# Optimization experiments

Hardware: AMD Instinct MI355X
Metric: run time of the kernel (lower is better)

Reference implementation:

```python
import math
import jax, jax.numpy as jnp
import numpy as np

B, T, C, H = 4, 2048, 1024, 16
HD = C // H

def gelu_tanh(x):
    return 0.5 * x * (1.0 + jnp.tanh(jnp.sqrt(2.0 / jnp.pi) * (x + 0.044715 * x * x * x)))

def layernorm(x, w, b, eps=1e-5):
    mu = jnp.mean(x, axis=-1, keepdims=True)
    var = jnp.var(x, axis=-1, keepdims=True)
    return (x - mu) * jax.lax.rsqrt(var + eps) * w + b

def setup_inputs() -> dict:
    key = jax.random.key(0)
    ks = jax.random.split(key, 8)
    s = 0.02
    return {
        "x": jax.random.normal(ks[0], (B, T, C), dtype=jnp.float32),
        "ln1_w": jnp.ones((C,), jnp.float32), "ln1_b": jnp.zeros((C,), jnp.float32),
        "attn_w": jax.random.normal(ks[1], (C, 3 * C), jnp.float32) * s,
        "attn_b": jnp.zeros((3 * C,), jnp.float32),
        "proj_w": jax.random.normal(ks[2], (C, C), jnp.float32) * s,
        "proj_b": jnp.zeros((C,), jnp.float32),
        "ln2_w": jnp.ones((C,), jnp.float32), "ln2_b": jnp.zeros((C,), jnp.float32),
        "fc_w": jax.random.normal(ks[3], (C, 4 * C), jnp.float32) * s,
        "fc_b": jnp.zeros((4 * C,), jnp.float32),
        "fc_proj_w": jax.random.normal(ks[4], (4 * C, C), jnp.float32) * s,
        "fc_proj_b": jnp.zeros((C,), jnp.float32),
    }

def block(x, ln1_w, ln1_b, attn_w, attn_b, proj_w, proj_b,
          ln2_w, ln2_b, fc_w, fc_b, fc_proj_w, fc_proj_b):
    # --- causal self-attention ---
    h = layernorm(x, ln1_w, ln1_b)
    qkv = h @ attn_w + attn_b                      # [B,T,3C]
    q, k, v = jnp.split(qkv, 3, axis=-1)
    q = q.reshape(B, T, H, HD).transpose(0, 2, 1, 3)  # [B,H,T,hd]
    k = k.reshape(B, T, H, HD).transpose(0, 2, 1, 3)
    v = v.reshape(B, T, H, HD).transpose(0, 2, 1, 3)
    att = jnp.einsum('bhqd,bhkd->bhqk', q, k) * (1.0 / math.sqrt(HD))
    mask = jnp.tril(jnp.ones((T, T), dtype=bool))
    att = jnp.where(mask, att, -jnp.inf)
    att = jax.nn.softmax(att, axis=-1)
    y = jnp.einsum('bhqk,bhkd->bhqd', att, v)
    y = y.transpose(0, 2, 1, 3).reshape(B, T, C)
    x = x + (y @ proj_w + proj_b)
    # --- MLP ---
    h = layernorm(x, ln2_w, ln2_b)
    h = gelu_tanh(h @ fc_w + fc_b)
    x = x + (h @ fc_proj_w + fc_proj_b)
    return x

def reference(x, ln1_w, ln1_b, attn_w, attn_b, proj_w, proj_b,
              ln2_w, ln2_b, fc_w, fc_b, fc_proj_w, fc_proj_b):
    return block(x, ln1_w, ln1_b, attn_w, attn_b, proj_w, proj_b,
                 ln2_w, ln2_b, fc_w, fc_b, fc_proj_w, fc_proj_b)
```

## Files before the change

### kernel.cpp

```cpp
#include <hip/hip_runtime.h>
#include <stdint.h>

#define TSEQ 2048
#define CDIM 1024
#define NHEAD 16
#define HDIM 64
#define NROWS 8192

typedef __bf16 bf16x8 __attribute__((ext_vector_type(8)));
typedef float f32x4 __attribute__((ext_vector_type(4)));
typedef float f32x16 __attribute__((ext_vector_type(16)));

__device__ __forceinline__ unsigned short f2bf(float f) {
  unsigned u = __builtin_bit_cast(unsigned, f);
  u = u + 0x7fffu + ((u >> 16) & 1u);
  return (unsigned short)(u >> 16);
}

__device__ __forceinline__ unsigned cvt_pk_bf16(float a, float b) {
  unsigned r;
  asm("v_cvt_pk_bf16_f32 %0, %1, %2" : "=v"(r) : "v"(a), "v"(b));
  return r;
}

__device__ __forceinline__ float gelu_f(float x) {
  float x3 = x * x * x;
  float z = 0.7978845608028654f * (x + 0.044715f * x3);
  float e = __expf(2.f * z);
  float t = 1.f - 2.f / (e + 1.f);
  return 0.5f * x * (1.f + t);
}

__device__ __forceinline__ void ldg_lds16(void* lds, const void* gsrc) {
  __builtin_amdgcn_global_load_lds(
      (__attribute__((address_space(1))) unsigned int*)(uintptr_t)gsrc,
      (__attribute__((address_space(3))) unsigned int*)lds,
      16, 0, 0);
}

__global__ __launch_bounds__(256) void k_wtrans(const float* __restrict__ W,
                                                unsigned short* __restrict__ Wt,
                                                int K, int N) {
  __shared__ unsigned short tl[32][40];
  int n0 = blockIdx.x * 32, k0 = blockIdx.y * 32;
  int tid = threadIdx.x;
  int r = tid >> 3, c4 = (tid & 7) * 4;
  float4 v = *(const float4*)(W + (size_t)(k0 + r) * N + n0 + c4);
  ushort4 o;
  o.x = f2bf(v.x); o.y = f2bf(v.y); o.z = f2bf(v.z); o.w = f2bf(v.w);
  *(ushort4*)&tl[r][c4] = o;
  __syncthreads();
  int n = tid >> 3, k4 = (tid & 7) * 4;
  ushort4 w;
  w.x = tl[k4 + 0][n]; w.y = tl[k4 + 1][n]; w.z = tl[k4 + 2][n]; w.w = tl[k4 + 3][n];
  *(ushort4*)(Wt + (size_t)(n0 + n) * K + k0 + k4) = w;
}

__global__ __launch_bounds__(256) void k_ln(const float* __restrict__ x,
                                            const float* __restrict__ w,
                                            const float* __restrict__ b,
                                            unsigned short* __restrict__ out) {
  int row = blockIdx.x;
  int tid = threadIdx.x;
  const float* xr = x + (size_t)row * CDIM;
  float4 v = *(const float4*)(xr + tid * 4);
  float s = v.x + v.y + v.z + v.w;
  float s2 = v.x * v.x + v.y * v.y + v.z * v.z + v.w * v.w;
#pragma unroll
  for (int off = 32; off; off >>= 1) {
    s += __shfl_xor(s, off);
    s2 += __shfl_xor(s2, off);
  }
  __shared__ float rbuf[8];
  int wv = tid >> 6, lane = tid & 63;
  if (lane == 0) { rbuf[wv] = s; rbuf[4 + wv] = s2; }
  __syncthreads();
  float S1 = rbuf[0] + rbuf[1] + rbuf[2] + rbuf[3];
  float S2 = rbuf[4] + rbuf[5] + rbuf[6] + rbuf[7];
  float mean = S1 * (1.f / CDIM);
  float var = S2 * (1.f / CDIM) - mean * mean;
  float rstd = rsqrtf(var + 1e-5f);
  float4 wv4 = *(const float4*)(w + tid * 4);
  float4 bv4 = *(const float4*)(b + tid * 4);
  ushort4 o;
  o.x = f2bf((v.x - mean) * rstd * wv4.x + bv4.x);
  o.y = f2bf((v.y - mean) * rstd * wv4.y + bv4.y);
  o.z = f2bf((v.z - mean) * rstd * wv4.z + bv4.z);
  o.w = f2bf((v.w - mean) * rstd * wv4.w + bv4.w);
  *(ushort4*)(out + (size_t)row * CDIM + tid * 4) = o;
}

template <int EPI>
__global__ __launch_bounds__(512, 4)
void k_gemm(const unsigned short* __restrict__ A,
            const unsigned short* __restrict__ Bt,
            const float* __restrict__ bias,
            const float* __restrict__ resid,
            void* __restrict__ Cout,
            int M, int N, int K) {
  constexpr int ABYTES = 128 * 64;
  constexpr int BBYTES = 256 * 64;
  constexpr int BUFSZ = ABYTES + BBYTES;
  __shared__ __align__(16) char lds[3 * BUFSZ];
  const int tid = threadIdx.x;
  const int wid = tid >> 6, lane = tid & 63;
  const int wm = wid >> 2, wn = wid & 3;
  const int fr = lane & 15, fq = lane >> 4;

  const int gx = gridDim.x;
  int flat = blockIdx.y * gx + blockIdx.x;
  {
    const int nwg = gx * gridDim.y;
    int q = nwg >> 3, r = nwg & 7;
    int xcd = flat & 7, idx = flat >> 3;
    flat = (xcd < r ? xcd * (q + 1) : r * (q + 1) + (xcd - r) * q) + idx;
  }
  const int bx = flat % gx, by = flat / gx;
  const long brow = (long)by * 128, bcol = (long)bx * 256;

  const int sby = (((lane & 3) ^ ((lane >> 3) & 3)) << 4);
  const char* gA = (const char*)(A + (size_t)(brow + wid * 16 + (lane >> 2)) * K) + sby;
  const char* gB = (const char*)(Bt + (size_t)(bcol + wid * 32 + (lane >> 2)) * K) + sby;

  const int NT = K >> 5;

#define STAGE_A(tt, bf)                                                 \
  ldg_lds16(lds + (bf) * BUFSZ + wid * 1024, gA + (size_t)(tt) * 64)
#define STAGE_B(tt, bf)                                                 \
  do {                                                                  \
    char* d_ = lds + (bf) * BUFSZ + ABYTES + wid * 2048;                \
    ldg_lds16(d_, gB + (size_t)(tt) * 64);                              \
    ldg_lds16(d_ + 1024, gB + (size_t)16 * K * 2 + (size_t)(tt) * 64);  \
  } while (0)

  STAGE_A(0, 0); STAGE_B(0, 0);
  STAGE_A(1, 1); STAGE_B(1, 1);

  f32x4 acc[4][4];
  const f32x4 vzero = {0.f, 0.f, 0.f, 0.f};
#pragma unroll
  for (int m = 0; m < 4; ++m)
#pragma unroll
    for (int n = 0; n < 4; ++n) acc[m][n] = vzero;

  const int ksw = ((fq ^ ((fr >> 1) & 3)) << 4);
  int buf = 0;
  for (int t = 0; t < NT; ++t) {
    if (t + 1 < NT) asm volatile("s_waitcnt vmcnt(3)" ::: "memory");
    else            asm volatile("s_waitcnt vmcnt(0)" ::: "memory");
    __builtin_amdgcn_s_barrier();
    __builtin_amdgcn_sched_barrier(0);
    const char* pA = lds + buf * BUFSZ;
    const char* pB = pA + ABYTES;
    int nbuf = buf + 2; if (nbuf >= 3) nbuf -= 3;
    if (t + 2 < NT) { STAGE_A(t + 2, nbuf); STAGE_B(t + 2, nbuf); }
    bf16x8 af[4], bfr[4];
#pragma unroll
    for (int m = 0; m < 4; ++m)
      af[m] = *(const bf16x8*)(pA + (wm * 64 + m * 16 + fr) * 64 + ksw);
#pragma unroll
    for (int n = 0; n < 4; ++n)
      bfr[n] = *(const bf16x8*)(pB + (wn * 64 + n * 16 + fr) * 64 + ksw);
    __builtin_amdgcn_s_setprio(1);
#pragma unroll
    for (int m = 0; m < 4; ++m)
#pragma unroll
      for (int n = 0; n < 4; ++n)
        acc[m][n] = __builtin_amdgcn_mfma_f32_16x16x32_bf16(af[m], bfr[n], acc[m][n], 0, 0, 0);
    __builtin_amdgcn_s_setprio(0);
    __builtin_amdgcn_sched_barrier(0);
    buf = buf + 1; if (buf == 3) buf = 0;
  }
#undef STAGE_A
#undef STAGE_B

#pragma unroll
  for (int m = 0; m < 4; ++m) {
    long row = brow + wm * 64 + m * 16 + fq * 4;
#pragma unroll
    for (int n = 0; n < 4; ++n) {
      long col = bcol + wn * 64 + n * 16 + fr;
      float bv = bias[col];
#pragma unroll
      for (int r = 0; r < 4; ++r) {
        float v = acc[m][n][r] + bv;
        long idx = (row + r) * (long)N + col;
        if (EPI == 0) {
          ((unsigned short*)Cout)[idx] = f2bf(v);
        } else if (EPI == 1) {
          ((unsigned short*)Cout)[idx] = f2bf(gelu_f(v));
        } else {
          ((float*)Cout)[idx] = v + resid[idx];
        }
      }
    }
  }
}

__global__ __launch_bounds__(256) void k_build_vt(const unsigned short* __restrict__ qkv,
                                                  unsigned short* __restrict__ vt) {
  __shared__ __align__(16) unsigned short tl[64][80];
  int bh = blockIdx.x, b = bh >> 4, h = bh & 15;
  int t0 = blockIdx.y * 64;
  int tid = threadIdx.x;
  int r = tid >> 2, cb = (tid & 3) * 16;
  const unsigned short* src =
      qkv + (size_t)(b * TSEQ + t0 + r) * (3 * CDIM) + 2 * CDIM + h * HDIM + cb;
  *(uint4*)&tl[r][cb] = *(const uint4*)src;
  *(uint4*)&tl[r][cb + 8] = *(const uint4*)(src + 8);
  __syncthreads();
  int d = tid >> 2, tb = (tid & 3) * 16;
  union { unsigned short u[16]; uint4 v[2]; } o;
#pragma unroll
  for (int j = 0; j < 16; ++j) o.u[j] = tl[tb + j][d];
  unsigned short* dst = vt + ((size_t)bh * HDIM + d) * TSEQ + t0 + tb;
  *(uint4*)dst = o.v[0];
  *(uint4*)(dst + 8) = o.v[1];
}

struct QSt {
  f32x16 OTlo, OThi;
  float m, l;
};

__device__ __forceinline__ void attn_qk_sm_pv(
    const bf16x8& k0, const bf16x8& k1, const bf16x8& k2, const bf16x8& k3,
    const bf16x8& v0, const bf16x8& v1, const bf16x8& v2, const bf16x8& v3,
    const bf16x8& q0f, const bf16x8& q1f, const bf16x8& q2f, const bf16x8& q3f,
    QSt& S, bool diag, int lq, int hi) {
  const float SC = 0.125f * 1.44269504088896f;
  f32x16 st;
#pragma unroll
  for (int r = 0; r < 16; ++r) st[r] = 0.f;
  st = __builtin_amdgcn_mfma_f32_32x32x16_bf16(k0, q0f, st, 0, 0, 0);
  st = __builtin_amdgcn_mfma_f32_32x32x16_bf16(k1, q1f, st, 0, 0, 0);
  st = __builtin_amdgcn_mfma_f32_32x32x16_bf16(k2, q2f, st, 0, 0, 0);
  st = __builtin_amdgcn_mfma_f32_32x32x16_bf16(k3, q3f, st, 0, 0, 0);
#pragma unroll
  for (int r = 0; r < 16; ++r) st[r] *= SC;
  if (diag) {
#pragma unroll
    for (int r = 0; r < 16; ++r) {
      int kvl = (r & 3) + 8 * (r >> 2) + 4 * hi;
      if (kvl > lq) st[r] = -1e30f;
    }
  }
  float tmax = st[0];
#pragma unroll
  for (int r = 1; r < 16; ++r) tmax = fmaxf(tmax, st[r]);
  float tm = fmaxf(tmax, __shfl_xor(tmax, 32));
  if (__any(tm > S.m + 8.f)) {
    float mnew = fmaxf(S.m, tm);
    float alpha = __builtin_amdgcn_exp2f(S.m - mnew);
    S.m = mnew;
    S.OTlo *= alpha;
    S.OThi *= alpha;
    S.l *= alpha;
  }
  unsigned c[8];
  float rs = 0.f;
#pragma unroll
  for (int i = 0; i < 8; ++i) {
    float pa = __builtin_amdgcn_exp2f(st[2 * i] - S.m);
    float pb = __builtin_amdgcn_exp2f(st[2 * i + 1] - S.m);
    rs += pa + pb;
    c[i] = cvt_pk_bf16(pa, pb);
  }
  S.l += rs + __shfl_xor(rs, 32);
  unsigned pc[8];
#pragma unroll
  for (int i = 0; i < 8; ++i) pc[i] = __shfl_xor(c[i], 32);
  uint4 w1, w2;
  w1.x = hi ? pc[2] : c[0]; w1.y = hi ? pc[3] : c[1];
  w1.z = hi ? c[2] : pc[0]; w1.w = hi ? c[3] : pc[1];
  w2.x = hi ? pc[6] : c[4]; w2.y = hi ? pc[7] : c[5];
  w2.z = hi ? c[6] : pc[4]; w2.w = hi ? c[7] : pc[5];
  bf16x8 f1 = __builtin_bit_cast(bf16x8, w1);
  bf16x8 f2 = __builtin_bit_cast(bf16x8, w2);
  S.OTlo = __builtin_amdgcn_mfma_f32_32x32x16_bf16(v0, f1, S.OTlo, 0, 0, 0);
  S.OTlo = __builtin_amdgcn_mfma_f32_32x32x16_bf16(v1, f2, S.OTlo, 0, 0, 0);
  S.OThi = __builtin_amdgcn_mfma_f32_32x32x16_bf16(v2, f1, S.OThi, 0, 0, 0);
  S.OThi = __builtin_amdgcn_mfma_f32_32x32x16_bf16(v3, f2, S.OThi, 0, 0, 0);
}

__global__ __launch_bounds__(256, 2) void k_attn(const unsigned short* __restrict__ qkv,
                                                 const unsigned short* __restrict__ vt,
                                                 unsigned short* __restrict__ y) {
  __shared__ __align__(16) unsigned short Ks[2][2048];
  __shared__ __align__(16) unsigned short Vs[2][2048];
  const int bh = blockIdx.x, b = bh >> 4, h = bh & 15;
  const int wv = threadIdx.x >> 6, lane = threadIdx.x & 63;
  const int by = blockIdx.y;
  const int w = by * 4 + wv;
  const int lq = lane & 31, hi = lane >> 5;
  const int ntL = w, ntH = 63 - w;
  const int q0L = w * 32, q0H = (63 - w) * 32;
  const int T = 64 - 4 * by;

  const unsigned short* qrowL = qkv + ((size_t)(b * TSEQ) + q0L + lq) * (3 * CDIM) + h * HDIM;
  const unsigned short* qrowH = qkv + ((size_t)(b * TSEQ) + q0H + lq) * (3 * CDIM) + h * HDIM;
  bf16x8 qL0 = *(const bf16x8*)(qrowL + 0 + hi * 8);
  bf16x8 qL1 = *(const bf16x8*)(qrowL + 16 + hi * 8);
  bf16x8 qL2 = *(const bf16x8*)(qrowL + 32 + hi * 8);
  bf16x8 qL3 = *(const bf16x8*)(qrowL + 48 + hi * 8);
  bf16x8 qH0 = *(const bf16x8*)(qrowH + 0 + hi * 8);
  bf16x8 qH1 = *(const bf16x8*)(qrowH + 16 + hi * 8);
  bf16x8 qH2 = *(const bf16x8*)(qrowH + 32 + hi * 8);
  bf16x8 qH3 = *(const bf16x8*)(qrowH + 48 + hi * 8);

  const int kr = lane & 31, kc = wv * 2 + (lane >> 5);
  const unsigned short* gK =
      qkv + ((size_t)(b * TSEQ) + kr) * (3 * CDIM) + CDIM + h * HDIM + kc * 8;
  const unsigned short* gV = vt + ((size_t)bh * HDIM + lane) * TSEQ + wv * 8;

#define STAGEKV(bf_, tt)                                                  \
  do {                                                                    \
    ldg_lds16((char*)Ks[bf_] + wv * 1024, gK + (size_t)(tt) * 32 * (3 * CDIM)); \
    ldg_lds16((char*)Vs[bf_] + wv * 1024, gV + (tt) * 32);                \
  } while (0)

  QSt SL, SH;
#pragma unroll
  for (int r = 0; r < 16; ++r) {
    SL.OTlo[r] = 0.f; SL.OThi[r] = 0.f; SH.OTlo[r] = 0.f; SH.OThi[r] = 0.f;
  }
  SL.m = -1e30f; SL.l = 0.f; SH.m = -1e30f; SH.l = 0.f;

  STAGEKV(0, 0);
  for (int t = 0; t < T; ++t) {
    __syncthreads();
    if (t + 1 < T) STAGEKV((t + 1) & 1, t + 1);
    if (t <= ntH) {
      const unsigned short* Kb = Ks[t & 1];
      const unsigned short* Vb = Vs[t & 1];
      bf16x8 k0 = *(const bf16x8*)(Kb + (0 + hi) * 256 + lq * 8);
      bf16x8 k1 = *(const bf16x8*)(Kb + (2 + hi) * 256 + lq * 8);
      bf16x8 k2 = *(const bf16x8*)(Kb + (4 + hi) * 256 + lq * 8);
      bf16x8 k3 = *(const bf16x8*)(Kb + (6 + hi) * 256 + lq * 8);
      bf16x8 v0 = *(const bf16x8*)(Vb + hi * 512 + lq * 8);
      bf16x8 v1 = *(const bf16x8*)(Vb + (2 + hi) * 512 + lq * 8);
      bf16x8 v2 = *(const bf16x8*)(Vb + hi * 512 + (lq + 32) * 8);
      bf16x8 v3 = *(const bf16x8*)(Vb + (2 + hi) * 512 + (lq + 32) * 8);
      attn_qk_sm_pv(k0, k1, k2, k3, v0, v1, v2, v3,
                    qH0, qH1, qH2, qH3, SH, t == ntH, lq, hi);
      if (t <= ntL)
        attn_qk_sm_pv(k0, k1, k2, k3, v0, v1, v2, v3,
                      qL0, qL1, qL2, qL3, SL, t == ntL, lq, hi);
    }
  }
#undef STAGEKV

  {
    float inv = 1.f / SH.l;
    unsigned short* yrow = y + ((size_t)(b * TSEQ) + q0H + lq) * CDIM + h * HDIM;
#pragma unroll
    for (int r = 0; r < 16; r += 2) {
      int d = (r & 3) + 8 * (r >> 2) + 4 * hi;
      unsigned lo0 = f2bf(SH.OTlo[r] * inv), lo1 = f2bf(SH.OTlo[r + 1] * inv);
      *(unsigned*)(yrow + d) = lo0 | (lo1 << 16);
      unsigned h0 = f2bf(SH.OThi[r] * inv), h1 = f2bf(SH.OThi[r + 1] * inv);
      *(unsigned*)(yrow + 32 + d) = h0 | (h1 << 16);
    }
  }
  {
    float inv = 1.f / SL.l;
    unsigned short* yrow = y + ((size_t)(b * TSEQ) + q0L + lq) * CDIM + h * HDIM;
#pragma unroll
    for (int r = 0; r < 16; r += 2) {
      int d = (r & 3) + 8 * (r >> 2) + 4 * hi;
      unsigned lo0 = f2bf(SL.OTlo[r] * inv), lo1 = f2bf(SL.OTlo[r + 1] * inv);
      *(unsigned*)(yrow + d) = lo0 | (lo1 << 16);
      unsigned h0 = f2bf(SL.OThi[r] * inv), h1 = f2bf(SL.OThi[r + 1] * inv);
      *(unsigned*)(yrow + 32 + d) = h0 | (h1 << 16);
    }
  }
}

extern "C" void kernel_launch(void* const* d_in, const int* in_sizes, int n_in,
                              void* d_out, int out_size, void* d_ws, size_t ws_size,
                              hipStream_t stream) {
  const float* x = (const float*)d_in[0];
  const float* ln1_w = (const float*)d_in[1];
  const float* ln1_b = (const float*)d_in[2];
  const float* attn_w = (const float*)d_in[3];
  const float* attn_b = (const float*)d_in[4];
  const float* proj_w = (const float*)d_in[5];
  const float* proj_b = (const float*)d_in[6];
  const float* ln2_w = (const float*)d_in[7];
  const float* ln2_b = (const float*)d_in[8];
  const float* fc_w = (const float*)d_in[9];
  const float* fc_b = (const float*)d_in[10];
  const float* fc_proj_w = (const float*)d_in[11];
  const float* fc_proj_b = (const float*)d_in[12];

  char* ws = (char*)d_ws;
  unsigned short* wt_attn = (unsigned short*)(ws + 0);
  unsigned short* wt_proj = (unsigned short*)(ws + 6291456);
  unsigned short* wt_fc = (unsigned short*)(ws + 8388608);
  unsigned short* wt_fcp = (unsigned short*)(ws + 16777216);
  float* x1 = (float*)(ws + 25165824);
  unsigned short* hbuf = (unsigned short*)(ws + 58720256);
  unsigned short* ybuf = (unsigned short*)(ws + 75497472);
  unsigned short* qkvb = (unsigned short*)(ws + 92274688);
  unsigned short* vtb = (unsigned short*)(ws + 142606336);
  unsigned short* gbuf = (unsigned short*)(ws + 92274688);

  k_wtrans<<<dim3(3072 / 32, 1024 / 32), 256, 0, stream>>>(attn_w, wt_attn, 1024, 3072);
  k_wtrans<<<dim3(1024 / 32, 1024 / 32), 256, 0, stream>>>(proj_w, wt_proj, 1024, 1024);
  k_wtrans<<<dim3(4096 / 32, 1024 / 32), 256, 0, stream>>>(fc_w, wt_fc, 1024, 4096);
  k_wtrans<<<dim3(1024 / 32, 4096 / 32), 256, 0, stream>>>(fc_proj_w, wt_fcp, 4096, 1024);

  k_ln<<<NROWS, 256, 0, stream>>>(x, ln1_w, ln1_b, hbuf);

  k_gemm<0><<<dim3(3072 / 256, NROWS / 128), 512, 0, stream>>>(
      hbuf, wt_attn, attn_b, nullptr, qkvb, NROWS, 3072, 1024);

  k_build_vt<<<dim3(64, TSEQ / 64), 256, 0, stream>>>(qkvb, vtb);

  k_attn<<<dim3(64, 8), 256, 0, stream>>>(qkvb, vtb, ybuf);

  k_gemm<2><<<dim3(1024 / 256, NROWS / 128), 512, 0, stream>>>(
      ybuf, wt_proj, proj_b, x, x1, NROWS, 1024, 1024);

  k_ln<<<NROWS, 256, 0, stream>>>(x1, ln2_w, ln2_b, hbuf);

  k_gemm<1><<<dim3(4096 / 256, NROWS / 128), 512, 0, stream>>>(
      hbuf, wt_fc, fc_b, nullptr, gbuf, NROWS, 4096, 1024);

  k_gemm<2><<<dim3(1024 / 256, NROWS / 128), 512, 0, stream>>>(
      gbuf, wt_fcp, fc_proj_b, x1, (float*)d_out, NROWS, 1024, 4096);
}
```

Before: 372.9 us.

## Stage two KV tiles per barrier in attention and raise MFMA wave priority

The attention loop now loads two 32-key K/V tiles per iteration into a doubled LDS double-buffer, which halves the number of __syncthreads barriers and deepens the prefetch. MFMA groups are also wrapped in s_setprio so that matrix issue from one wave is favoured over the softmax work of other waves. LDS use doubles to 32KB per block, which may affect occupancy at two blocks per CU. T is always even, so the paired tiles stay in bounds.

```diff
diff --git a/kernel.cpp b/kernel.cpp
--- a/kernel.cpp
+++ b/kernel.cpp
@@ -232,10 +232,12 @@
   f32x16 st;
 #pragma unroll
   for (int r = 0; r < 16; ++r) st[r] = 0.f;
+  __builtin_amdgcn_s_setprio(1);
   st = __builtin_amdgcn_mfma_f32_32x32x16_bf16(k0, q0f, st, 0, 0, 0);
   st = __builtin_amdgcn_mfma_f32_32x32x16_bf16(k1, q1f, st, 0, 0, 0);
   st = __builtin_amdgcn_mfma_f32_32x32x16_bf16(k2, q2f, st, 0, 0, 0);
   st = __builtin_amdgcn_mfma_f32_32x32x16_bf16(k3, q3f, st, 0, 0, 0);
+  __builtin_amdgcn_s_setprio(0);
 #pragma unroll
   for (int r = 0; r < 16; ++r) st[r] *= SC;
   if (diag) {
@@ -277,17 +279,19 @@
   w2.z = hi ? c[6] : pc[4]; w2.w = hi ? c[7] : pc[5];
   bf16x8 f1 = __builtin_bit_cast(bf16x8, w1);
   bf16x8 f2 = __builtin_bit_cast(bf16x8, w2);
+  __builtin_amdgcn_s_setprio(1);
   S.OTlo = __builtin_amdgcn_mfma_f32_32x32x16_bf16(v0, f1, S.OTlo, 0, 0, 0);
   S.OTlo = __builtin_amdgcn_mfma_f32_32x32x16_bf16(v1, f2, S.OTlo, 0, 0, 0);
   S.OThi = __builtin_amdgcn_mfma_f32_32x32x16_bf16(v2, f1, S.OThi, 0, 0, 0);
   S.OThi = __builtin_amdgcn_mfma_f32_32x32x16_bf16(v3, f2, S.OThi, 0, 0, 0);
+  __builtin_amdgcn_s_setprio(0);
 }
 
 __global__ __launch_bounds__(256, 2) void k_attn(const unsigned short* __restrict__ qkv,
                                                  const unsigned short* __restrict__ vt,
                                                  unsigned short* __restrict__ y) {
-  __shared__ __align__(16) unsigned short Ks[2][2048];
-  __shared__ __align__(16) unsigned short Vs[2][2048];
+  __shared__ __align__(16) unsigned short Ks[2][2][2048];
+  __shared__ __align__(16) unsigned short Vs[2][2][2048];
   const int bh = blockIdx.x, b = bh >> 4, h = bh & 15;
   const int wv = threadIdx.x >> 6, lane = threadIdx.x & 63;
   const int by = blockIdx.y;
@@ -313,10 +317,12 @@
       qkv + ((size_t)(b * TSEQ) + kr) * (3 * CDIM) + CDIM + h * HDIM + kc * 8;
   const unsigned short* gV = vt + ((size_t)bh * HDIM + lane) * TSEQ + wv * 8;
 
-#define STAGEKV(bf_, tt)                                                  \
-  do {                                                                    \
-    ldg_lds16((char*)Ks[bf_] + wv * 1024, gK + (size_t)(tt) * 32 * (3 * CDIM)); \
-    ldg_lds16((char*)Vs[bf_] + wv * 1024, gV + (tt) * 32);                \
+#define STAGEKV2(pb, tt)                                                       \
+  do {                                                                         \
+    ldg_lds16((char*)Ks[pb][0] + wv * 1024, gK + (size_t)(tt) * 32 * (3 * CDIM));     \
+    ldg_lds16((char*)Vs[pb][0] + wv * 1024, gV + (size_t)(tt) * 32);           \
+    ldg_lds16((char*)Ks[pb][1] + wv * 1024, gK + (size_t)(tt + 1) * 32 * (3 * CDIM)); \
+    ldg_lds16((char*)Vs[pb][1] + wv * 1024, gV + (size_t)(tt + 1) * 32);       \
   } while (0)
 
   QSt SL, SH;
@@ -326,29 +332,34 @@
   }
   SL.m = -1e30f; SL.l = 0.f; SH.m = -1e30f; SH.l = 0.f;
 
-  STAGEKV(0, 0);
-  for (int t = 0; t < T; ++t) {
+  STAGEKV2(0, 0);
+  for (int tt = 0; tt < T; tt += 2) {
     __syncthreads();
-    if (t + 1 < T) STAGEKV((t + 1) & 1, t + 1);
-    if (t <= ntH) {
-      const unsigned short* Kb = Ks[t & 1];
-      const unsigned short* Vb = Vs[t & 1];
-      bf16x8 k0 = *(const bf16x8*)(Kb + (0 + hi) * 256 + lq * 8);
-      bf16x8 k1 = *(const bf16x8*)(Kb + (2 + hi) * 256 + lq * 8);
-      bf16x8 k2 = *(const bf16x8*)(Kb + (4 + hi) * 256 + lq * 8);
-      bf16x8 k3 = *(const bf16x8*)(Kb + (6 + hi) * 256 + lq * 8);
-      bf16x8 v0 = *(const bf16x8*)(Vb + hi * 512 + lq * 8);
-      bf16x8 v1 = *(const bf16x8*)(Vb + (2 + hi) * 512 + lq * 8);
-      bf16x8 v2 = *(const bf16x8*)(Vb + hi * 512 + (lq + 32) * 8);
-      bf16x8 v3 = *(const bf16x8*)(Vb + (2 + hi) * 512 + (lq + 32) * 8);
-      attn_qk_sm_pv(k0, k1, k2, k3, v0, v1, v2, v3,
-                    qH0, qH1, qH2, qH3, SH, t == ntH, lq, hi);
-      if (t <= ntL)
+    const int pb = (tt >> 1) & 1;
+    if (tt + 2 < T) STAGEKV2(pb ^ 1, tt + 2);
+#pragma unroll
+    for (int sub = 0; sub < 2; ++sub) {
+      const int t = tt + sub;
+      if (t <= ntH) {
+        const unsigned short* Kb = Ks[pb][sub];
+        const unsigned short* Vb = Vs[pb][sub];
+        bf16x8 k0 = *(const bf16x8*)(Kb + (0 + hi) * 256 + lq * 8);
+        bf16x8 k1 = *(const bf16x8*)(Kb + (2 + hi) * 256 + lq * 8);
+        bf16x8 k2 = *(const bf16x8*)(Kb + (4 + hi) * 256 + lq * 8);
+        bf16x8 k3 = *(const bf16x8*)(Kb + (6 + hi) * 256 + lq * 8);
+        bf16x8 v0 = *(const bf16x8*)(Vb + hi * 512 + lq * 8);
+        bf16x8 v1 = *(const bf16x8*)(Vb + (2 + hi) * 512 + lq * 8);
+        bf16x8 v2 = *(const bf16x8*)(Vb + hi * 512 + (lq + 32) * 8);
+        bf16x8 v3 = *(const bf16x8*)(Vb + (2 + hi) * 512 + (lq + 32) * 8);
         attn_qk_sm_pv(k0, k1, k2, k3, v0, v1, v2, v3,
-                      qL0, qL1, qL2, qL3, SL, t == ntL, lq, hi);
+                      qH0, qH1, qH2, qH3, SH, t == ntH, lq, hi);
+        if (t <= ntL)
+          attn_qk_sm_pv(k0, k1, k2, k3, v0, v1, v2, v3,
+                        qL0, qL1, qL2, qL3, SL, t == ntL, lq, hi);
+      }
     }
   }
-#undef STAGEKV
+#undef STAGEKV2
 
   {
     float inv = 1.f / SH.l;
```

Result: no change. 367.0 us (-1.6%).
